# Kernel tuning notes

Hardware: AMD Instinct MI355X
Metric: run time of the kernel (lower is better)

Reference implementation:

```python
import jax, jax.numpy as jnp
import numpy as np

D_MODEL = 768
NHEAD = 12
HEAD_DIM = D_MODEL // NHEAD
WINDOW = 33  # band half-width = 16


def setup_inputs() -> dict:
    key = jax.random.key(0)
    ks = jax.random.split(key, 9)
    B, T, C = 2, 4096, D_MODEL
    s = 0.02
    return {
        "x": jax.random.normal(ks[0], (B, T, C), jnp.float32),
        "Wq": jax.random.normal(ks[1], (C, C), jnp.float32) * s,
        "bq": jnp.zeros((C,), jnp.float32),
        "Wk": jax.random.normal(ks[2], (C, C), jnp.float32) * s,
        "bk": jnp.zeros((C,), jnp.float32),
        "Wv": jax.random.normal(ks[3], (C, C), jnp.float32) * s,
        "bv": jnp.zeros((C,), jnp.float32),
        "Wo": jax.random.normal(ks[4], (C, C), jnp.float32) * s,
        "bo": jnp.zeros((C,), jnp.float32),
    }


def reference(x, Wq, bq, Wk, bk, Wv, bv, Wo, bo):
    B, T, C = x.shape
    H, D = NHEAD, HEAD_DIM
    scale = D ** -0.5
    # torch Linear: x @ W.T + b
    q = (x @ Wq.T + bq).reshape(B, T, H, D).transpose(0, 2, 1, 3)  # [B,H,T,D]
    k = (x @ Wk.T + bk).reshape(B, T, H, D).transpose(0, 2, 1, 3)
    v = (x @ Wv.T + bv).reshape(B, T, H, D).transpose(0, 2, 1, 3)
    scores = jnp.einsum("bhqd,bhkd->bhqk", q, k) * scale  # [B,H,T,T]
    idx = jnp.arange(T)
    local_mask = jnp.abs(idx[:, None] - idx[None, :]) <= (WINDOW // 2)  # [T,T]
    scores = jnp.where(local_mask[None, None], scores, -jnp.inf)
    attn = jax.nn.softmax(scores, axis=-1)  # dropout=0 / eval mode
    out = jnp.einsum("bhqk,bhkd->bhqd", attn, v)  # [B,H,T,D]
    out = out.transpose(0, 2, 1, 3).reshape(B, T, C)
    return out @ Wo.T + bo
```

## Files before the change

### kernel.cpp

```cpp
#include <hip/hip_runtime.h>
#include <math.h>
#include <cstdint>
#include <cstddef>

typedef unsigned short u16;
typedef short bf16x8 __attribute__((ext_vector_type(8)));
typedef float f32x4 __attribute__((ext_vector_type(4)));
typedef u16 u16x8 __attribute__((ext_vector_type(8)));
typedef u16 u16x4 __attribute__((ext_vector_type(4)));

#define T_LEN 4096
#define NH 12
#define HD 64
#define DMODEL 768
#define GK 768
#define QKV_STRIDE 6291456ul

__device__ __forceinline__ u16 f2bf(float x) {
  union { float f; unsigned u; } v; v.f = x;
  unsigned r = v.u + 0x7fffu + ((v.u >> 16) & 1u);
  return (u16)(r >> 16);
}

__device__ __forceinline__ void async16(const u16* g, u16* l) {
  __builtin_amdgcn_global_load_lds(
      (const __attribute__((address_space(1))) unsigned int*)g,
      (__attribute__((address_space(3))) unsigned int*)l, 16, 0, 0);
}

__global__ void cvt_all(const float* __restrict__ x,
                        const float* __restrict__ Wq, const float* __restrict__ Wk,
                        const float* __restrict__ Wv, const float* __restrict__ Wo,
                        u16* __restrict__ xb, u16* __restrict__ wqkv, u16* __restrict__ wo_b) {
  int bx = blockIdx.x;
  const float* s; u16* d; int base;
  if (bx < 6144)      { s = x;  d = xb;             base = bx; }
  else if (bx < 6720) { s = Wq; d = wqkv;           base = bx - 6144; }
  else if (bx < 7296) { s = Wk; d = wqkv + 589824;  base = bx - 6720; }
  else if (bx < 7872) { s = Wv; d = wqkv + 1179648; base = bx - 7296; }
  else                { s = Wo; d = wo_b;           base = bx - 7872; }
  int i = (base * 256 + (int)threadIdx.x) * 4;
  float4 v = *(const float4*)(s + i);
  u16x4 o;
  o[0] = f2bf(v.x); o[1] = f2bf(v.y); o[2] = f2bf(v.z); o[3] = f2bf(v.w);
  *(u16x4*)(d + i) = o;
}

#define BN 128
#define BK 32
#define CPAD 8

template <int EPI, int MI, int NX>
__global__ __launch_bounds__(256)
void gemm_bt(const u16* __restrict__ A, const u16* __restrict__ B,
             const float* __restrict__ bias0, const float* __restrict__ bias1,
             void* __restrict__ outp) {
  constexpr int BMt = MI * 32;
  constexpr int PER = NX / 8;
  __shared__ __align__(16) u16 As[BMt * BK];
  __shared__ __align__(16) u16 Bs[BN * BK];
  __shared__ __align__(16) u16 Cs[EPI == 0 ? BMt * (BN + CPAD) : 8];

  const int bid  = blockIdx.x;
  const int xcd  = bid & 7;
  const int slot = bid >> 3;
  const int bx   = xcd * PER + (slot % PER);
  const int by   = slot / PER;

  const int tid  = threadIdx.x;
  const int lane = tid & 63;
  const int wave = tid >> 6;
  const int wm = wave & 1, wn = wave >> 1;
  const long am0 = (long)bx * BMt;
  const long bn0 = (long)by * BN;
  const int r16 = lane & 15;
  const int kh  = lane >> 4;
  const int sw8 = (kh ^ ((r16 >> 1) & 3)) * 8;

  f32x4 acc[MI][4] = {};

  const int srow   = lane >> 2;
  const int schunk = ((lane & 3) ^ ((lane >> 3) & 3)) * 8;
  const u16* Ag = A + (am0 + wave * 16 + srow) * GK + schunk;
  const u16* Bg = B + (bn0 + wave * 16 + srow) * GK + schunk;
  u16* Bl0 = &Bs[(wave * 16) * BK];
  u16* Bl1 = &Bs[(64 + wave * 16) * BK];

  for (int kt = 0; kt < GK; kt += BK) {
    __syncthreads();
#pragma unroll
    for (int s = 0; s < MI / 2; s++)
      async16(Ag + (size_t)(s * 64) * GK + kt, &As[(s * 64 + wave * 16) * BK]);
    async16(Bg + kt, Bl0);
    async16(Bg + 64 * GK + kt, Bl1);
    __syncthreads();
    bf16x8 af[MI], bfr[4];
#pragma unroll
    for (int i = 0; i < MI; i++)
      af[i] = *(const bf16x8*)&As[(wm * MI * 16 + i * 16 + r16) * BK + sw8];
#pragma unroll
    for (int j = 0; j < 4; j++)
      bfr[j] = *(const bf16x8*)&Bs[(wn * 64 + j * 16 + r16) * BK + sw8];
#pragma unroll
    for (int i = 0; i < MI; i++)
#pragma unroll
      for (int j = 0; j < 4; j++)
        acc[i][j] = __builtin_amdgcn_mfma_f32_16x16x32_bf16(af[i], bfr[j], acc[i][j], 0, 0, 0);
  }

  const int m0 = (int)am0 + wm * MI * 16;

  if (EPI == 0) {
    const int tens = (int)(bn0 >= 768);
    const int c0 = (int)bn0 - tens * 768;
    const float* bp = tens ? bias1 : bias0;
    u16* outb = (u16*)outp + (size_t)tens * QKV_STRIDE;
#pragma unroll
    for (int j = 0; j < 4; j++) {
      int lc = wn * 64 + j * 16 + r16;
      float bv = bp[c0 + lc];
#pragma unroll
      for (int i = 0; i < MI; i++) {
        int lr = wm * MI * 16 + i * 16 + kh * 4;
#pragma unroll
        for (int r = 0; r < 4; r++)
          Cs[(lr + r) * (BN + CPAD) + lc] = f2bf(acc[i][j][r] + bv);
      }
    }
    __syncthreads();
#pragma unroll
    for (int z = 0; z < BMt / 16; z++) {
      int cidx = z * 256 + tid;
      int row = cidx >> 4, ch = (cidx & 15) * 8;
      uint4 val = *(const uint4*)&Cs[row * (BN + CPAD) + ch];
      *(uint4*)(outb + (size_t)(am0 + row) * DMODEL + c0 + ch) = val;
    }
  } else if (EPI == 2) {
    u16* vtb = (u16*)outp;
    const int kr = kh * 4;
#pragma unroll
    for (int j = 0; j < 4; j++) {
      int cl = (int)bn0 + wn * 64 + j * 16;
      int hj = cl >> 6;
      int dlane = (cl & 63) + r16;
      float bv = bias0[cl + r16];
#pragma unroll
      for (int i = 0; i < MI; i++) {
        int row0 = m0 + i * 16;
        int b_ = row0 >> 12;
        int tb = (row0 & 4095) >> 4;
        size_t base = (((size_t)(b_ * NH + hj) * 256 + tb) << 10) + dlane * 16 + kr;
        u16x4 pk;
#pragma unroll
        for (int r = 0; r < 4; r++) pk[r] = f2bf(acc[i][j][r] + bv);
        *(u16x4*)(vtb + base) = pk;
      }
    }
  } else {
    float* O = (float*)outp;
#pragma unroll
    for (int i = 0; i < MI; i++) {
#pragma unroll
      for (int r = 0; r < 4; r++) {
        int row = m0 + i * 16 + kh * 4 + r;
        float* orow = O + (size_t)row * DMODEL;
#pragma unroll
        for (int j = 0; j < 4; j++) {
          int col = (int)bn0 + wn * 64 + j * 16 + r16;
          orow[col] = acc[i][j][r] + bias0[col];
        }
      }
    }
  }
}

#define PSS 72

__global__ __launch_bounds__(256)
void attn_mfma(const u16* __restrict__ qkv, const u16* __restrict__ vt,
               u16* __restrict__ attn) {
  __shared__ __align__(16) u16 Ps[4][16 * PSS];
  const int tid = threadIdx.x, lane = tid & 63, wave = tid >> 6;
  const int r16 = lane & 15, quad = lane >> 4;
  const int q0 = blockIdx.x * 64;
  const int h = blockIdx.y, b = blockIdx.z;
  const long rowbase = (long)b * T_LEN;
  const int hc = h * HD;
  const u16* Qg = qkv;
  const u16* Kg = qkv + QKV_STRIDE;
  const u16* Vh = vt + ((size_t)(b * NH + h)) * (256 * 1024);

  const int qbase = q0 + wave * 16;
  const int kb = qbase - 16;

  const u16* qrow = Qg + (rowbase + qbase + r16) * DMODEL + hc + quad * 8;
  bf16x8 qa0 = *(const bf16x8*)qrow;
  bf16x8 qa1 = *(const bf16x8*)(qrow + 32);

  f32x4 s[3];
#pragma unroll
  for (int t = 0; t < 3; t++) {
    const u16* krow = Kg + (rowbase + kb + t * 16 + r16) * DMODEL + hc + quad * 8;
    bf16x8 kf0 = *(const bf16x8*)krow;
    bf16x8 kf1 = *(const bf16x8*)(krow + 32);
    f32x4 a = {};
    a = __builtin_amdgcn_mfma_f32_16x16x32_bf16(qa0, kf0, a, 0, 0, 0);
    a = __builtin_amdgcn_mfma_f32_16x16x32_bf16(qa1, kf1, a, 0, 0, 0);
    s[t] = a;
  }

  float pr[3][4];
#pragma unroll
  for (int r = 0; r < 4; r++) {
    const int qg = qbase + quad * 4 + r;
    float sc[3];
#pragma unroll
    for (int t = 0; t < 3; t++) {
      int key = kb + t * 16 + r16;
      bool ok = (key >= qg - 16) && (key <= qg + 16) && (key >= 0) && (key < T_LEN);
      sc[t] = ok ? s[t][r] * 0.125f : -INFINITY;
    }
    float mx = fmaxf(sc[0], fmaxf(sc[1], sc[2]));
    mx = fmaxf(mx, __shfl_xor(mx, 1));
    mx = fmaxf(mx, __shfl_xor(mx, 2));
    mx = fmaxf(mx, __shfl_xor(mx, 4));
    mx = fmaxf(mx, __shfl_xor(mx, 8));
    float e0 = __expf(sc[0] - mx), e1 = __expf(sc[1] - mx), e2 = __expf(sc[2] - mx);
    float l = e0 + e1 + e2;
    l += __shfl_xor(l, 1);
    l += __shfl_xor(l, 2);
    l += __shfl_xor(l, 4);
    l += __shfl_xor(l, 8);
    float inv = 1.0f / l;
    pr[0][r] = e0 * inv; pr[1][r] = e1 * inv; pr[2][r] = e2 * inv;
  }

  u16* psw = &Ps[wave][0];
#pragma unroll
  for (int t = 0; t < 3; t++)
#pragma unroll
    for (int r = 0; r < 4; r++)
      psw[(quad * 4 + r) * PSS + t * 16 + r16] = f2bf(pr[t][r]);
#pragma unroll
  for (int r = 0; r < 4; r++)
    psw[(quad * 4 + r) * PSS + 48 + r16] = 0;

  bf16x8 pa0 = *(const bf16x8*)&psw[r16 * PSS + quad * 8];
  bf16x8 pa1 = *(const bf16x8*)&psw[r16 * PSS + 32 + quad * 8];

  const int kq1 = kb + quad * 8;
  const int kq2 = kb + 32 + quad * 8;
  const int o1 = (kq1 >> 4) * 1024 + (kq1 & 15);
  const int o2 = (kq2 >> 4) * 1024 + (kq2 & 15);
  f32x4 o[4];
#pragma unroll
  for (int c = 0; c < 4; c++) {
    const u16* vb = Vh + (16 * c + r16) * 16;
    bf16x8 v1 = *(const bf16x8*)(vb + o1);
    bf16x8 v2 = *(const bf16x8*)(vb + o2);
    f32x4 a = {};
    a = __builtin_amdgcn_mfma_f32_16x16x32_bf16(pa0, v1, a, 0, 0, 0);
    a = __builtin_amdgcn_mfma_f32_16x16x32_bf16(pa1, v2, a, 0, 0, 0);
    o[c] = a;
  }

#pragma unroll
  for (int c = 0; c < 4; c++)
#pragma unroll
    for (int r = 0; r < 4; r++)
      psw[(quad * 4 + r) * PSS + 16 * c + r16] = f2bf(o[c][r]);
  {
    int rr = lane >> 3, cc = (lane & 7) * 8;
    u16x8 v0 = *(const u16x8*)&psw[rr * PSS + cc];
    u16x8 v1 = *(const u16x8*)&psw[(8 + rr) * PSS + cc];
    u16* ob = attn + (rowbase + qbase) * DMODEL + hc;
    *(u16x8*)(ob + (size_t)rr * DMODEL + cc) = v0;
    *(u16x8*)(ob + (size_t)(8 + rr) * DMODEL + cc) = v1;
  }
}

extern "C" void kernel_launch(void* const* d_in, const int* in_sizes, int n_in,
                              void* d_out, int out_size, void* d_ws, size_t ws_size,
                              hipStream_t stream) {
  const float* x  = (const float*)d_in[0];
  const float* Wq = (const float*)d_in[1];
  const float* bq = (const float*)d_in[2];
  const float* Wk = (const float*)d_in[3];
  const float* bk = (const float*)d_in[4];
  const float* Wv = (const float*)d_in[5];
  const float* bv = (const float*)d_in[6];
  const float* Wo = (const float*)d_in[7];
  const float* bo = (const float*)d_in[8];
  float* out = (float*)d_out;
  char* ws = (char*)d_ws;

  u16* xb   = (u16*)(ws);
  u16* wqkv = (u16*)(ws + 12582912);
  u16* wo_b = (u16*)(ws + 16121856);
  u16* qkv  = (u16*)(ws + 17301504);
  u16* attnb = (u16*)(ws + 55050240);

  cvt_all<<<8448, 256, 0, stream>>>(x, Wq, Wk, Wv, Wo, xb, wqkv, wo_b);

  gemm_bt<0, 4, 64><<<768, 256, 0, stream>>>(xb, wqkv, bq, bk, (void*)qkv);
  gemm_bt<2, 4, 64><<<384, 256, 0, stream>>>(xb, wqkv + 1179648, bv, bv,
                                             (void*)(qkv + 2 * QKV_STRIDE));
  attn_mfma<<<dim3(64, 12, 2), 256, 0, stream>>>(qkv, qkv + 2 * QKV_STRIDE, attnb);
  gemm_bt<1, 2, 128><<<768, 256, 0, stream>>>(attnb, wo_b, bo, bo, (void*)out);
}
```

Measured before the change: 168.9 us.

## Double-buffer GEMM K loop, merge QKV GEMMs, stage output via LDS, add setprio

The GEMM main loop now double-buffers the A/B tiles, so the async loads for the next K step are issued before the current step's MFMAs, with one barrier per step. The Q/K and V projection launches are merged into one 1152-block launch whose epilogue branches on column range. The fp32 output-projection epilogue is staged through LDS so global writes become coalesced float4 stores. The attention MFMAs are wrapped in s_setprio. The changes target load latency, launch overhead and uncoalesced stores, at the cost of more LDS per block and possibly lower occupancy.

```diff
diff --git a/kernel.cpp b/kernel.cpp
--- a/kernel.cpp
+++ b/kernel.cpp
@@ -54,12 +54,17 @@
 __global__ __launch_bounds__(256)
 void gemm_bt(const u16* __restrict__ A, const u16* __restrict__ B,
              const float* __restrict__ bias0, const float* __restrict__ bias1,
-             void* __restrict__ outp) {
+             const float* __restrict__ bias2, void* __restrict__ outp) {
   constexpr int BMt = MI * 32;
   constexpr int PER = NX / 8;
-  __shared__ __align__(16) u16 As[BMt * BK];
-  __shared__ __align__(16) u16 Bs[BN * BK];
-  __shared__ __align__(16) u16 Cs[EPI == 0 ? BMt * (BN + CPAD) : 8];
+  constexpr int NSTEP = GK / BK;
+  constexpr int STG = 2 * (BMt + BN) * BK * 2;
+  constexpr int CSZ = (EPI == 3) ? BMt * (BN + CPAD) * 2
+                                 : 64 * 132 * 4;
+  constexpr int SMEM = STG > CSZ ? STG : CSZ;
+  __shared__ __align__(16) char smem[SMEM];
+  u16* AsB = (u16*)smem;
+  u16* BsB = (u16*)smem + 2 * BMt * BK;
 
   const int bid  = blockIdx.x;
   const int xcd  = bid & 7;
@@ -83,93 +88,112 @@
   const int schunk = ((lane & 3) ^ ((lane >> 3) & 3)) * 8;
   const u16* Ag = A + (am0 + wave * 16 + srow) * GK + schunk;
   const u16* Bg = B + (bn0 + wave * 16 + srow) * GK + schunk;
-  u16* Bl0 = &Bs[(wave * 16) * BK];
-  u16* Bl1 = &Bs[(64 + wave * 16) * BK];
-
-  for (int kt = 0; kt < GK; kt += BK) {
-    __syncthreads();
-#pragma unroll
-    for (int s = 0; s < MI / 2; s++)
-      async16(Ag + (size_t)(s * 64) * GK + kt, &As[(s * 64 + wave * 16) * BK]);
-    async16(Bg + kt, Bl0);
-    async16(Bg + 64 * GK + kt, Bl1);
-    __syncthreads();
+
+  auto stage = [&](int buf, int kt) {
+    u16* Ab = AsB + buf * (BMt * BK);
+    u16* Bb = BsB + buf * (BN * BK);
+#pragma unroll
+    for (int s2 = 0; s2 < MI / 2; s2++)
+      async16(Ag + (size_t)(s2 * 64) * GK + kt, &Ab[(s2 * 64 + wave * 16) * BK]);
+    async16(Bg + kt, &Bb[(wave * 16) * BK]);
+    async16(Bg + (size_t)64 * GK + kt, &Bb[(64 + wave * 16) * BK]);
+  };
+
+  stage(0, 0);
+  __syncthreads();
+  for (int s = 0; s < NSTEP; ++s) {
+    const int cur = s & 1;
+    if (s + 1 < NSTEP) stage(cur ^ 1, (s + 1) * BK);
+    const u16* Ac = AsB + cur * (BMt * BK);
+    const u16* Bc = BsB + cur * (BN * BK);
     bf16x8 af[MI], bfr[4];
 #pragma unroll
     for (int i = 0; i < MI; i++)
-      af[i] = *(const bf16x8*)&As[(wm * MI * 16 + i * 16 + r16) * BK + sw8];
+      af[i] = *(const bf16x8*)&Ac[(wm * MI * 16 + i * 16 + r16) * BK + sw8];
 #pragma unroll
     for (int j = 0; j < 4; j++)
-      bfr[j] = *(const bf16x8*)&Bs[(wn * 64 + j * 16 + r16) * BK + sw8];
+      bfr[j] = *(const bf16x8*)&Bc[(wn * 64 + j * 16 + r16) * BK + sw8];
 #pragma unroll
     for (int i = 0; i < MI; i++)
 #pragma unroll
       for (int j = 0; j < 4; j++)
         acc[i][j] = __builtin_amdgcn_mfma_f32_16x16x32_bf16(af[i], bfr[j], acc[i][j], 0, 0, 0);
+    __syncthreads();
   }
 
   const int m0 = (int)am0 + wm * MI * 16;
 
-  if (EPI == 0) {
-    const int tens = (int)(bn0 >= 768);
-    const int c0 = (int)bn0 - tens * 768;
-    const float* bp = tens ? bias1 : bias0;
-    u16* outb = (u16*)outp + (size_t)tens * QKV_STRIDE;
+  if (EPI == 3) {
+    if (bn0 < 1536) {
+      const int tens = (int)(bn0 >= 768);
+      const int c0 = (int)bn0 - tens * 768;
+      const float* bp = tens ? bias1 : bias0;
+      u16* outb = (u16*)outp + (size_t)tens * QKV_STRIDE;
+      u16* Cs = (u16*)smem;
+#pragma unroll
+      for (int j = 0; j < 4; j++) {
+        int lc = wn * 64 + j * 16 + r16;
+        float bv = bp[c0 + lc];
+#pragma unroll
+        for (int i = 0; i < MI; i++) {
+          int lr = wm * MI * 16 + i * 16 + kh * 4;
+#pragma unroll
+          for (int r = 0; r < 4; r++)
+            Cs[(lr + r) * (BN + CPAD) + lc] = f2bf(acc[i][j][r] + bv);
+        }
+      }
+      __syncthreads();
+#pragma unroll
+      for (int z = 0; z < BMt / 16; z++) {
+        int cidx = z * 256 + tid;
+        int row = cidx >> 4, ch = (cidx & 15) * 8;
+        uint4 val = *(const uint4*)&Cs[row * (BN + CPAD) + ch];
+        *(uint4*)(outb + (size_t)(am0 + row) * DMODEL + c0 + ch) = val;
+      }
+    } else {
+      u16* vtb = (u16*)outp + 2 * QKV_STRIDE;
+      const int kr = kh * 4;
+#pragma unroll
+      for (int j = 0; j < 4; j++) {
+        int cl = (int)(bn0 - 1536) + wn * 64 + j * 16;
+        int hj = cl >> 6;
+        int dlane = (cl & 63) + r16;
+        float bv = bias2[cl + r16];
+#pragma unroll
+        for (int i = 0; i < MI; i++) {
+          int row0 = m0 + i * 16;
+          int b_ = row0 >> 12;
+          int tb = (row0 & 4095) >> 4;
+          size_t base = (((size_t)(b_ * NH + hj) * 256 + tb) << 10) + dlane * 16 + kr;
+          u16x4 pk;
+#pragma unroll
+          for (int r = 0; r < 4; r++) pk[r] = f2bf(acc[i][j][r] + bv);
+          *(u16x4*)(vtb + base) = pk;
+        }
+      }
+    }
+  } else {
+    float* Cf = (float*)smem;
 #pragma unroll
     for (int j = 0; j < 4; j++) {
       int lc = wn * 64 + j * 16 + r16;
-      float bv = bp[c0 + lc];
+      float bv = bias0[(int)bn0 + lc];
 #pragma unroll
       for (int i = 0; i < MI; i++) {
         int lr = wm * MI * 16 + i * 16 + kh * 4;
 #pragma unroll
         for (int r = 0; r < 4; r++)
-          Cs[(lr + r) * (BN + CPAD) + lc] = f2bf(acc[i][j][r] + bv);
+          Cf[(lr + r) * 132 + lc] = acc[i][j][r] + bv;
       }
     }
     __syncthreads();
-#pragma unroll
-    for (int z = 0; z < BMt / 16; z++) {
-      int cidx = z * 256 + tid;
-      int row = cidx >> 4, ch = (cidx & 15) * 8;
-      uint4 val = *(const uint4*)&Cs[row * (BN + CPAD) + ch];
-      *(uint4*)(outb + (size_t)(am0 + row) * DMODEL + c0 + ch) = val;
-    }
-  } else if (EPI == 2) {
-    u16* vtb = (u16*)outp;
-    const int kr = kh * 4;
-#pragma unroll
-    for (int j = 0; j < 4; j++) {
-      int cl = (int)bn0 + wn * 64 + j * 16;
-      int hj = cl >> 6;
-      int dlane = (cl & 63) + r16;
-      float bv = bias0[cl + r16];
-#pragma unroll
-      for (int i = 0; i < MI; i++) {
-        int row0 = m0 + i * 16;
-        int b_ = row0 >> 12;
-        int tb = (row0 & 4095) >> 4;
-        size_t base = (((size_t)(b_ * NH + hj) * 256 + tb) << 10) + dlane * 16 + kr;
-        u16x4 pk;
-#pragma unroll
-        for (int r = 0; r < 4; r++) pk[r] = f2bf(acc[i][j][r] + bv);
-        *(u16x4*)(vtb + base) = pk;
-      }
-    }
-  } else {
     float* O = (float*)outp;
 #pragma unroll
-    for (int i = 0; i < MI; i++) {
-#pragma unroll
-      for (int r = 0; r < 4; r++) {
-        int row = m0 + i * 16 + kh * 4 + r;
-        float* orow = O + (size_t)row * DMODEL;
-#pragma unroll
-        for (int j = 0; j < 4; j++) {
-          int col = (int)bn0 + wn * 64 + j * 16 + r16;
-          orow[col] = acc[i][j][r] + bias0[col];
-        }
-      }
+    for (int z = 0; z < 8; z++) {
+      int idx = z * 256 + tid;
+      int row = idx >> 5, c4 = (idx & 31) * 4;
+      float4 v = *(const float4*)&Cf[row * 132 + c4];
+      *(float4*)(O + (size_t)(am0 + row) * DMODEL + bn0 + c4) = v;
     }
   }
 }
@@ -204,8 +228,10 @@
     bf16x8 kf0 = *(const bf16x8*)krow;
     bf16x8 kf1 = *(const bf16x8*)(krow + 32);
     f32x4 a = {};
+    __builtin_amdgcn_s_setprio(1);
     a = __builtin_amdgcn_mfma_f32_16x16x32_bf16(qa0, kf0, a, 0, 0, 0);
     a = __builtin_amdgcn_mfma_f32_16x16x32_bf16(qa1, kf1, a, 0, 0, 0);
+    __builtin_amdgcn_s_setprio(0);
     s[t] = a;
   }
 
@@ -259,8 +285,10 @@
     bf16x8 v1 = *(const bf16x8*)(vb + o1);
     bf16x8 v2 = *(const bf16x8*)(vb + o2);
     f32x4 a = {};
+    __builtin_amdgcn_s_setprio(1);
     a = __builtin_amdgcn_mfma_f32_16x16x32_bf16(pa0, v1, a, 0, 0, 0);
     a = __builtin_amdgcn_mfma_f32_16x16x32_bf16(pa1, v2, a, 0, 0, 0);
+    __builtin_amdgcn_s_setprio(0);
     o[c] = a;
   }
 
@@ -302,9 +330,7 @@
 
   cvt_all<<<8448, 256, 0, stream>>>(x, Wq, Wk, Wv, Wo, xb, wqkv, wo_b);
 
-  gemm_bt<0, 4, 64><<<768, 256, 0, stream>>>(xb, wqkv, bq, bk, (void*)qkv);
-  gemm_bt<2, 4, 64><<<384, 256, 0, stream>>>(xb, wqkv + 1179648, bv, bv,
-                                             (void*)(qkv + 2 * QKV_STRIDE));
+  gemm_bt<3, 4, 64><<<1152, 256, 0, stream>>>(xb, wqkv, bq, bk, bv, (void*)qkv);
   attn_mfma<<<dim3(64, 12, 2), 256, 0, stream>>>(qkv, qkv + 2 * QKV_STRIDE, attnb);
-  gemm_bt<1, 2, 128><<<768, 256, 0, stream>>>(attnb, wo_b, bo, bo, (void*)out);
-}
+  gemm_bt<1, 2, 128><<<768, 256, 0, stream>>>(attnb, wo_b, bo, bo, bo, (void*)out);
+}
```

After: 174.9 us. 3.6% more time.
